# Optimization experiments

Measured on AMD Instinct MI355X. Metric: run time of the kernel, lower is better.

The kernel has to match this reference:

```python
import jax, jax.numpy as jnp
import numpy as np

S, T, B = 32, 64, 64          # sentences, tokens/sentence, batch
V, E, H, G, C = 32000, 128, 128, 128, 5  # vocab, embed, intra hid, inter hid, classes


def _gru_dir(x, h0, Wih, Whh, bih, bhh):
    # x: [T,B,D]; Wih: [3H,D]; Whh: [3H,H]  (PyTorch GRU gate order r,z,n)
    xg = jnp.einsum('tbd,gd->tbg', x, Wih) + bih  # precompute input gates [T,B,3H]
    def step(h, xt):
        gh = h @ Whh.T + bhh
        ir, iz, inn = jnp.split(xt, 3, axis=-1)
        hr, hz, hn = jnp.split(gh, 3, axis=-1)
        r = jax.nn.sigmoid(ir + hr)
        z = jax.nn.sigmoid(iz + hz)
        n = jnp.tanh(inn + r * hn)
        hnew = (1 - z) * n + z * h
        return hnew, hnew
    _, out = jax.lax.scan(step, h0, xg)
    return out  # [T,B,H]


def _bigru(x, Wih, Whh, bih, bhh):
    # x: [T,B,D]; Wih: [2,3H,D] (fwd, bwd). Zero initial state (init_hidden()).
    h0 = jnp.zeros((x.shape[1], Whh.shape[-1]), x.dtype)
    of = _gru_dir(x, h0, Wih[0], Whh[0], bih[0], bhh[0])
    ob = _gru_dir(x[::-1], h0, Wih[1], Whh[1], bih[1], bhh[1])[::-1]
    return jnp.concatenate([of, ob], axis=-1)  # [T,B,2H]


def setup_inputs() -> dict:
    key = jax.random.key(0)
    ks = iter(jax.random.split(key, 20))
    u = lambda k, shp, s: jax.random.uniform(k, shp, jnp.float32, -s, s)
    tokens = jax.random.randint(next(ks), (S, T, B), 0, V)
    return {
        'tokens': tokens,
        'embed_table': jax.random.normal(next(ks), (V, E), jnp.float32),
        # intra biGRU (input E, hidden H)
        'Wih_intra': u(next(ks), (2, 3 * H, E), 0.08),
        'Whh_intra': u(next(ks), (2, 3 * H, H), 0.08),
        'bih_intra': u(next(ks), (2, 3 * H), 0.08),
        'bhh_intra': u(next(ks), (2, 3 * H), 0.08),
        # intra attention
        'W_W_intra': u(next(ks), (2 * H, 2 * H), 0.1),
        'b_intra': u(next(ks), (2 * H,), 0.1),
        'proj_intra': u(next(ks), (2 * H,), 0.1),
        # inter biGRU (input 2H, hidden G)
        'Wih_inter': u(next(ks), (2, 3 * G, 2 * H), 0.08),
        'Whh_inter': u(next(ks), (2, 3 * G, G), 0.08),
        'bih_inter': u(next(ks), (2, 3 * G), 0.08),
        'bhh_inter': u(next(ks), (2, 3 * G), 0.08),
        # inter attention
        'W_W_inter': u(next(ks), (2 * G, 2 * G), 0.1),
        'b_inter': u(next(ks), (2 * G,), 0.1),
        'proj_inter': u(next(ks), (2 * G,), 0.1),
        # final linear
        'W_final': u(next(ks), (C, 2 * G), 0.06),
        'b_final': u(next(ks), (C,), 0.06),
    }


def reference(tokens, embed_table, Wih_intra, Whh_intra, bih_intra, bhh_intra,
              W_W_intra, b_intra, proj_intra, Wih_inter, Whh_inter, bih_inter,
              bhh_inter, W_W_inter, b_inter, proj_inter, W_final, b_final):
    # ---- intra (word-level) per sentence, fresh zero state each sentence ----
    emb = embed_table[tokens]                                   # [S,T,B,E]
    intra_out = jax.vmap(
        lambda xs: _bigru(xs, Wih_intra, Whh_intra, bih_intra, bhh_intra)
    )(emb)                                                      # [S,T,B,2H]
    u1 = jnp.tanh(jnp.einsum('stbh,hk->stbk', intra_out, W_W_intra) + b_intra)
    a1 = jnp.einsum('stbk,k->stb', u1, proj_intra)              # [S,T,B]
    a1 = jax.nn.softmax(a1, axis=1)                             # softmax over tokens
    sent_vecs = jnp.einsum('stb,stbh->sbh', a1, intra_out)      # [S,B,2H]
    # ---- inter (sentence-level) ----
    inter_out = _bigru(sent_vecs, Wih_inter, Whh_inter, bih_inter, bhh_inter)  # [S,B,2G]
    u2 = jnp.tanh(jnp.einsum('sbh,hk->sbk', inter_out, W_W_inter) + b_inter)
    a2 = jnp.einsum('sbk,k->sb', u2, proj_inter)                # NO softmax (faithful to source)
    doc_vec = jnp.einsum('sb,sbh->bh', a2, inter_out)           # [B,2G]
    final_map = doc_vec @ W_final.T + b_final                   # [B,C]
    return final_map
```

## Files before the change

kernel.cpp:

```cpp
#include <hip/hip_runtime.h>

#define S_ 32
#define T_ 64
#define B_ 64
#define V_ 32000
#define E_ 128
#define H_ 128
#define G_ 128
#define C_ 5

typedef short s8v __attribute__((ext_vector_type(8)));
typedef __bf16 b8v __attribute__((ext_vector_type(8)));
typedef float f32x4 __attribute__((ext_vector_type(4)));

template <typename V>
__device__ inline auto mfma_sel(V a, V b, f32x4 c, int)
    -> decltype(__builtin_amdgcn_mfma_f32_16x16x32_bf16(a, b, c, 0, 0, 0)) {
  return __builtin_amdgcn_mfma_f32_16x16x32_bf16(a, b, c, 0, 0, 0);
}
template <typename V>
__device__ inline f32x4 mfma_sel(V a, V b, f32x4 c, long) {
  return __builtin_amdgcn_mfma_f32_16x16x32_bf16(
      __builtin_bit_cast(b8v, a), __builtin_bit_cast(b8v, b), c, 0, 0, 0);
}
__device__ inline f32x4 mfma16(s8v a, s8v b, f32x4 c) { return mfma_sel(a, b, c, 0); }

__device__ inline float b2f(unsigned short u) {
  union { unsigned int i; float f; } v; v.i = ((unsigned int)u) << 16; return v.f;
}
__device__ inline unsigned short f2b(float f) {
  union { float f; unsigned int i; } v; v.f = f;
  return (unsigned short)((v.i + 0x8000u) >> 16);
}
__device__ inline unsigned short f2b_rne(float f) {
  union { float f; unsigned int i; } v; v.f = f;
  unsigned int r = (v.i + 0x7fffu + ((v.i >> 16) & 1u)) >> 16;
  return (unsigned short)r;
}
__device__ inline s8v cvt8(const float* p) {
  const float4 a = *(const float4*)p;
  const float4 b = *(const float4*)(p + 4);
  s8v r;
  r[0] = (short)f2b_rne(a.x); r[1] = (short)f2b_rne(a.y);
  r[2] = (short)f2b_rne(a.z); r[3] = (short)f2b_rne(a.w);
  r[4] = (short)f2b_rne(b.x); r[5] = (short)f2b_rne(b.y);
  r[6] = (short)f2b_rne(b.z); r[7] = (short)f2b_rne(b.w);
  return r;
}
__device__ inline float fsigm(float x) {
  return __builtin_amdgcn_rcpf(1.f + __builtin_amdgcn_exp2f(-1.44269504f * x));
}
__device__ inline float ftanh(float x) {
  return 1.f - 2.f * __builtin_amdgcn_rcpf(1.f + __builtin_amdgcn_exp2f(2.88539008f * x));
}

__device__ inline void lds_barrier() {
  asm volatile("s_waitcnt lgkmcnt(0)\n\ts_barrier" ::: "memory");
}

__global__ __launch_bounds__(256) void k_gtab(
    const float* __restrict__ emb,
    const float* __restrict__ wih,
    const float* __restrict__ bih,
    const float* __restrict__ bhh,
    const float* __restrict__ wwi,
    const float* __restrict__ wihI,
    unsigned short* __restrict__ gtab,
    unsigned short* __restrict__ wta,
    unsigned short* __restrict__ wib)
{
  __shared__ __align__(16) unsigned short smem[64 * 264];
  const int bid = blockIdx.x, tid = threadIdx.x;
  if (bid >= 504) {
    const int cb = bid - 504;
    for (int i = 0; i < 48; ++i) {
      int e4 = cb * 12288 + i * 256 + tid;
      float4 v = *(const float4*)&wihI[(size_t)e4 * 4];
      ushort4 u;
      u.x = f2b_rne(v.x); u.y = f2b_rne(v.y); u.z = f2b_rne(v.z); u.w = f2b_rne(v.w);
      *(ushort4*)&wib[(size_t)e4 * 4] = u;
    }
    return;
  }
  if (bid >= 500) {
    const int n0 = (bid - 500) * 64;
    for (int i = 0; i < 64; ++i) {
      int cid = i * 256 + tid;
      int k = cid >> 6, nl = cid & 63;
      smem[nl * 264 + k] = f2b_rne(wwi[k * 256 + n0 + nl]);
    }
    __syncthreads();
    for (int i = 0; i < 8; ++i) {
      int cid = i * 256 + tid;
      int nl = cid >> 5, k8 = cid & 31;
      *(int4*)&wta[(size_t)(n0 + nl) * 256 + k8 * 8] =
          *(const int4*)&smem[nl * 264 + k8 * 8];
    }
    return;
  }
  const int vbase = bid * 64;
  for (int i = 0; i < 8; ++i) {
    int cid = i * 256 + tid;
    int row = cid >> 5, kc = cid & 31;
    float4 v = *(const float4*)&emb[(size_t)(vbase + row) * 128 + kc * 4];
    ushort4 u;
    u.x = f2b_rne(v.x); u.y = f2b_rne(v.y); u.z = f2b_rne(v.z); u.w = f2b_rne(v.w);
    *(ushort4*)&smem[row * 136 + kc * 4] = u;
  }
  __syncthreads();
  const int w = tid >> 6, l = tid & 63, q = l >> 4, ln = l & 15;
  s8v af[4][4];
  for (int mt = 0; mt < 4; ++mt)
    for (int kf = 0; kf < 4; ++kf)
      af[mt][kf] = *(const s8v*)&smem[(mt * 16 + ln) * 136 + kf * 32 + q * 8];
  for (int nchunk = 0; nchunk < 6; ++nchunk) {
    const int nbase = nchunk * 128;
    s8v bf[2][4];
    float bias[2];
    for (int nt = 0; nt < 2; ++nt) {
      int c = nbase + (w * 2 + nt) * 16 + ln;
      int g = (c < 384) ? c : (c - 384);
      bias[nt] = bih[c] + (g < 256 ? bhh[c] : 0.f);
      for (int kf = 0; kf < 4; ++kf)
        bf[nt][kf] = cvt8(&wih[(size_t)c * 128 + kf * 32 + q * 8]);
    }
    for (int mt = 0; mt < 4; ++mt) {
      for (int nt = 0; nt < 2; ++nt) {
        f32x4 acc = {0.f, 0.f, 0.f, 0.f};
        for (int kf = 0; kf < 4; ++kf) acc = mfma16(af[mt][kf], bf[nt][kf], acc);
        const int col = nbase + (w * 2 + nt) * 16 + ln;
        for (int r = 0; r < 4; ++r) {
          const int row = vbase + mt * 16 + q * 4 + r;
          gtab[(size_t)row * 768 + col] = f2b_rne(acc[r] + bias[nt]);
        }
      }
    }
  }
}

__global__ __launch_bounds__(512) void k_intra(
    const int* __restrict__ tokens,
    const unsigned short* __restrict__ gtab,
    const float* __restrict__ whh,
    const float* __restrict__ bhh,
    unsigned short* __restrict__ iout)
{
  const int bid = blockIdx.x;
  const int s = bid >> 3, dir = (bid >> 2) & 1, bq = bid & 3;
  const int bbase = bq * 16;
  const int tid = threadIdx.x;
  const int w = tid >> 6, l = tid & 63, q = l >> 4, ln = l & 15;
  const int gbase = w * 16, g0 = gbase + q * 4;

  __shared__ __align__(16) unsigned short hb[2][16 * 136];
  __shared__ int tokl[T_ * 16];

  for (int i = tid; i < 2 * 16 * 136; i += 512) ((unsigned short*)hb)[i] = 0;
  for (int i = tid; i < T_ * 16; i += 512) {
    int t = i >> 4, bl = i & 15;
    tokl[i] = tokens[(s * T_ + t) * B_ + bbase + bl] * 768 + dir * 384;
  }

  s8v af[3][4];
  float hbn[4];
  const float* whd = whh + (size_t)dir * (384 * 128);
  const float* bhd = bhh + dir * 384;
  for (int g3 = 0; g3 < 3; ++g3) {
    const int R = g3 * 128 + gbase;
    for (int kf = 0; kf < 4; ++kf)
      af[g3][kf] = cvt8(&whd[(size_t)(R + ln) * 128 + kf * 32 + q * 8]);
  }
  for (int r = 0; r < 4; ++r) hbn[r] = bhd[256 + gbase + q * 4 + r];
  float h[4] = {0.f, 0.f, 0.f, 0.f};
  const int b = bbase + ln;
  __syncthreads();

  ushort4 Xr[4], Xz[4], Xn[4];
#define GLOAD_I(slot, st)                                                   \
  do {                                                                      \
    int tt_ = (st) > (T_ - 1) ? (T_ - 1) : (st);                            \
    int tg_ = dir ? (T_ - 1 - tt_) : tt_;                                   \
    const unsigned short* gp_ =                                             \
        gtab + (size_t)(tokl[tg_ * 16 + ln] + g0);                          \
    Xr[slot] = *(const ushort4*)&gp_[0];                                    \
    Xz[slot] = *(const ushort4*)&gp_[128];                                  \
    Xn[slot] = *(const ushort4*)&gp_[256];                                  \
  } while (0)

  GLOAD_I(0, 0);
  GLOAD_I(1, 1);
  GLOAD_I(2, 2);

  int p = 0;
  for (int it = 0; it < T_ / 4; ++it) {
#pragma unroll
    for (int j = 0; j < 4; ++j) {
      const int step = it * 4 + j;
      const int t = dir ? (T_ - 1 - step) : step;
      GLOAD_I((j + 3) & 3, step + 3);

      s8v bfr[4];
      for (int kf = 0; kf < 4; ++kf)
        bfr[kf] = *(const s8v*)&hb[p][ln * 136 + kf * 32 + q * 8];
      f32x4 c0 = {0.f, 0.f, 0.f, 0.f}, c1 = c0, c2 = c0;
      for (int kf = 0; kf < 4; ++kf) {
        c0 = mfma16(af[0][kf], bfr[kf], c0);
        c1 = mfma16(af[1][kf], bfr[kf], c1);
        c2 = mfma16(af[2][kf], bfr[kf], c2);
      }

      const unsigned short* xrp = (const unsigned short*)&Xr[j];
      const unsigned short* xzp = (const unsigned short*)&Xz[j];
      const unsigned short* xnp = (const unsigned short*)&Xn[j];
      unsigned short hnb[4];
      for (int r = 0; r < 4; ++r) {
        float rr = fsigm(b2f(xrp[r]) + c0[r]);
        float zz = fsigm(b2f(xzp[r]) + c1[r]);
        float nn = ftanh(b2f(xnp[r]) + rr * (c2[r] + hbn[r]));
        float hv = zz * (h[r] - nn) + nn;
        h[r] = hv;
        hnb[r] = f2b(hv);
      }
      ushort4 hv4; hv4.x = hnb[0]; hv4.y = hnb[1]; hv4.z = hnb[2]; hv4.w = hnb[3];
      *(ushort4*)&hb[p ^ 1][ln * 136 + g0] = hv4;
      *(ushort4*)&iout[((size_t)(s * T_ + t) * B_ + b) * 256 + dir * 128 + g0] = hv4;
      lds_barrier();
      p ^= 1;
    }
  }
#undef GLOAD_I
}

__global__ __launch_bounds__(512, 1) void k_attn(
    const unsigned short* __restrict__ iout,
    const unsigned short* __restrict__ wta,
    const float* __restrict__ bint,
    const float* __restrict__ proj,
    const unsigned short* __restrict__ wib,
    const float* __restrict__ bihI,
    const float* __restrict__ bhhI,
    float* __restrict__ xgi)
{
  __shared__ __align__(16) unsigned short wlds[256 * 256];
  __shared__ float lgbuf[8][16];
  __shared__ float lbuf[8][8];
  const int tid = threadIdx.x, bid = blockIdx.x;
  const int s = bid >> 3, b0 = (bid & 7) * 8;
  for (int i = 0; i < 16; ++i) {
    int cid = i * 512 + tid;
    int n = cid >> 5, kc = cid & 31;
    *(int4*)&wlds[n * 256 + ((kc ^ (n & 15)) << 3)] =
        *(const int4*)&wta[(size_t)n * 256 + kc * 8];
  }
  const int w = tid >> 6, l = tid & 63, q = l >> 4, ln = l & 15;
  float bbv[16], ppv[16];
  for (int nt = 0; nt < 16; ++nt) {
    bbv[nt] = bint[nt * 16 + ln];
    ppv[nt] = proj[nt * 16 + ln];
  }
  __syncthreads();

  float O[8][8];
  for (int kf = 0; kf < 8; ++kf)
    for (int j = 0; j < 8; ++j) O[kf][j] = 0.f;
  float l_acc = 0.f;

  for (int tile = 0; tile < 4; ++tile) {
    const int t = (w * 4 + tile) * 2 + (ln >> 3);
    const size_t row = (size_t)((s * T_ + t) * B_ + b0 + (ln & 7));
    s8v af[8];
    for (int kf = 0; kf < 8; ++kf)
      af[kf] = *(const s8v*)&iout[row * 256 + kf * 32 + q * 8];
    float p0 = 0.f, p1 = 0.f, p2 = 0.f, p3 = 0.f;
    for (int nt = 0; nt < 16; ++nt) {
      f32x4 c = {0.f, 0.f, 0.f, 0.f};
      for (int kf = 0; kf < 8; ++kf) {
        s8v bf = *(const s8v*)&wlds[(nt * 16 + ln) * 256 + (((kf * 4 + q) ^ ln) << 3)];
        c = mfma16(af[kf], bf, c);
      }
      p0 += ppv[nt] * ftanh(c[0] + bbv[nt]);
      p1 += ppv[nt] * ftanh(c[1] + bbv[nt]);
      p2 += ppv[nt] * ftanh(c[2] + bbv[nt]);
      p3 += ppv[nt] * ftanh(c[3] + bbv[nt]);
    }
    for (int d = 1; d < 16; d <<= 1) {
      p0 += __shfl_xor(p0, d); p1 += __shfl_xor(p1, d);
      p2 += __shfl_xor(p2, d); p3 += __shfl_xor(p3, d);
    }
    if (ln == 0) {
      lgbuf[w][q * 4 + 0] = p0; lgbuf[w][q * 4 + 1] = p1;
      lgbuf[w][q * 4 + 2] = p2; lgbuf[w][q * 4 + 3] = p3;
    }
    const float lg = lgbuf[w][ln];
    const float e = __builtin_amdgcn_exp2f(1.44269504f * lg);
    l_acc += e;
    for (int kf = 0; kf < 8; ++kf)
      for (int j = 0; j < 8; ++j)
        O[kf][j] += e * b2f((unsigned short)af[kf][j]);
  }
  l_acc += __shfl_xor(l_acc, 8);
  for (int kf = 0; kf < 8; ++kf)
    for (int j = 0; j < 8; ++j) O[kf][j] += __shfl_xor(O[kf][j], 8);
  __syncthreads();
  float* obuf = (float*)wlds;
  unsigned short* svl = (unsigned short*)(((char*)wlds) + 65536);
  if (ln < 8) {
    const int base = w * 2048 + ln * 256 + q * 8;
    for (int kf = 0; kf < 8; ++kf) {
      float4 v0; v0.x = O[kf][0]; v0.y = O[kf][1]; v0.z = O[kf][2]; v0.w = O[kf][3];
      float4 v1; v1.x = O[kf][4]; v1.y = O[kf][5]; v1.z = O[kf][6]; v1.w = O[kf][7];
      *(float4*)&obuf[base + kf * 32]     = v0;
      *(float4*)&obuf[base + kf * 32 + 4] = v1;
    }
    if (q == 0) lbuf[w][ln] = l_acc;
  }
  {
    ushort4 z4; z4.x = 0; z4.y = 0; z4.z = 0; z4.w = 0;
    int rr = 8 + (tid >> 6), cc = (tid & 63) * 4;
    *(ushort4*)&svl[rr * 264 + cc] = z4;
  }
  __syncthreads();
  const int idx = tid * 4;
  const int bb_ = idx >> 8;
  float4 acc; acc.x = 0.f; acc.y = 0.f; acc.z = 0.f; acc.w = 0.f;
  float lsum = 0.f;
  for (int w8 = 0; w8 < 8; ++w8) {
    const float4 v = *(const float4*)&obuf[w8 * 2048 + idx];
    acc.x += v.x; acc.y += v.y; acc.z += v.z; acc.w += v.w;
    lsum += lbuf[w8][bb_];
  }
  const float inv = __builtin_amdgcn_rcpf(lsum);
  ushort4 u;
  u.x = f2b_rne(acc.x * inv); u.y = f2b_rne(acc.y * inv);
  u.z = f2b_rne(acc.z * inv); u.w = f2b_rne(acc.w * inv);
  *(ushort4*)&svl[bb_ * 264 + (idx & 255)] = u;
  __syncthreads();
  s8v afx[8];
  for (int kf = 0; kf < 8; ++kf)
    afx[kf] = *(const s8v*)&svl[ln * 264 + kf * 32 + q * 8];
  for (int nt = 0; nt < 6; ++nt) {
    const int c = w * 96 + nt * 16 + ln;
    const int dirI = (c >= 384) ? 1 : 0;
    const int g = c - dirI * 384;
    const float biasx = bihI[c] + (g < 256 ? bhhI[c] : 0.f);
    f32x4 cacc = {0.f, 0.f, 0.f, 0.f};
    for (int kf = 0; kf < 8; ++kf) {
      s8v bfx = *(const s8v*)&wib[(size_t)c * 256 + kf * 32 + q * 8];
      cacc = mfma16(afx[kf], bfx, cacc);
    }
    if (q < 2) {
      for (int r = 0; r < 4; ++r) {
        const int m = q * 4 + r;
        xgi[((size_t)dirI * 2048 + s * B_ + b0 + m) * 384 + g] = cacc[r] + biasx;
      }
    }
  }
}

__global__ __launch_bounds__(512) void k_inter(
    const float* __restrict__ xgi,
    const float* __restrict__ whh,
    const float* __restrict__ bhh,
    float* __restrict__ io2)
{
  const int bid = blockIdx.x;
  const int dir = bid >> 2, bq = bid & 3, bbase = bq * 16;
  const int tid = threadIdx.x;
  const int w = tid >> 6, l = tid & 63, q = l >> 4, ln = l & 15;
  const int gbase = w * 16, g0 = gbase + q * 4;
  __shared__ __align__(16) unsigned short hb[2][16 * 136];
  for (int i = tid; i < 2 * 16 * 136; i += 512) ((unsigned short*)hb)[i] = 0;
  s8v af[3][4];
  float hbn[4];
  const float* whd = whh + (size_t)dir * (384 * 128);
  const float* bhd = bhh + dir * 384;
  for (int g3 = 0; g3 < 3; ++g3) {
    const int R = g3 * 128 + gbase;
    for (int kf = 0; kf < 4; ++kf)
      af[g3][kf] = cvt8(&whd[(size_t)(R + ln) * 128 + kf * 32 + q * 8]);
  }
  for (int r = 0; r < 4; ++r) hbn[r] = bhd[256 + gbase + q * 4 + r];
  float h[4] = {0.f, 0.f, 0.f, 0.f};
  const int b = bbase + ln;
  __syncthreads();

  float4 Vr[4], Vz[4], Vn[4];
#define GLOAD_S(slot, st)                                                   \
  do {                                                                      \
    int tt_ = (st) > (S_ - 1) ? (S_ - 1) : (st);                            \
    int sg_ = dir ? (S_ - 1 - tt_) : tt_;                                   \
    const float* xp_ = xgi + ((size_t)dir * 2048 + sg_ * 64 + b) * 384 + g0;\
    Vr[slot] = *(const float4*)&xp_[0];                                     \
    Vz[slot] = *(const float4*)&xp_[128];                                   \
    Vn[slot] = *(const float4*)&xp_[256];                                   \
  } while (0)

  GLOAD_S(0, 0);
  GLOAD_S(1, 1);
  GLOAD_S(2, 2);

  int p = 0;
  for (int it = 0; it < S_ / 4; ++it) {
#pragma unroll
    for (int j = 0; j < 4; ++j) {
      const int step = it * 4 + j;
      const int sI = dir ? (S_ - 1 - step) : step;
      GLOAD_S((j + 3) & 3, step + 3);

      s8v bfr[4];
      for (int kf = 0; kf < 4; ++kf)
        bfr[kf] = *(const s8v*)&hb[p][ln * 136 + kf * 32 + q * 8];
      f32x4 c0 = {0.f, 0.f, 0.f, 0.f}, c1 = c0, c2 = c0;
      for (int kf = 0; kf < 4; ++kf) {
        c0 = mfma16(af[0][kf], bfr[kf], c0);
        c1 = mfma16(af[1][kf], bfr[kf], c1);
        c2 = mfma16(af[2][kf], bfr[kf], c2);
      }
      const float irv[4] = {Vr[j].x, Vr[j].y, Vr[j].z, Vr[j].w};
      const float izv[4] = {Vz[j].x, Vz[j].y, Vz[j].z, Vz[j].w};
      const float inv[4] = {Vn[j].x, Vn[j].y, Vn[j].z, Vn[j].w};
      unsigned short hnb[4];
      for (int r = 0; r < 4; ++r) {
        float rr = fsigm(irv[r] + c0[r]);
        float zz = fsigm(izv[r] + c1[r]);
        float nn = ftanh(inv[r] + rr * (c2[r] + hbn[r]));
        float hv = zz * (h[r] - nn) + nn;
        h[r] = hv;
        hnb[r] = f2b(hv);
      }
      ushort4 hv4; hv4.x = hnb[0]; hv4.y = hnb[1]; hv4.z = hnb[2]; hv4.w = hnb[3];
      *(ushort4*)&hb[p ^ 1][ln * 136 + g0] = hv4;
      float4 of4; of4.x = h[0]; of4.y = h[1]; of4.z = h[2]; of4.w = h[3];
      *(float4*)&io2[((size_t)(sI * 64 + b)) * 256 + dir * 128 + g0] = of4;
      lds_barrier();
      p ^= 1;
    }
  }
#undef GLOAD_S
}

__global__ __launch_bounds__(256) void k_attn_i(
    const float* __restrict__ io2,
    const float* __restrict__ wwI,
    const float* __restrict__ bI,
    const float* __restrict__ projI,
    float* __restrict__ a2)
{
  const int bid = blockIdx.x, tid = threadIdx.x;
  const int r0 = bid * 8;
  __shared__ float iol[8 * 256];
  __shared__ float red[4 * 8];
  for (int i = 0; i < 8; ++i) iol[i * 256 + tid] = io2[(size_t)(r0 + i) * 256 + tid];
  __syncthreads();
  float acc[8];
  for (int i = 0; i < 8; ++i) acc[i] = 0.f;
  for (int hh = 0; hh < 256; ++hh) {
    const float wv = wwI[hh * 256 + tid];
    for (int i = 0; i < 8; ++i) acc[i] += wv * iol[i * 256 + hh];
  }
  const float bb = bI[tid], pp = projI[tid];
  float p[8];
  for (int i = 0; i < 8; ++i) p[i] = pp * ftanh(acc[i] + bb);
  for (int d = 1; d < 64; d <<= 1)
    for (int i = 0; i < 8; ++i) p[i] += __shfl_xor(p[i], d);
  const int w = tid >> 6, l = tid & 63;
  if (l == 0)
    for (int i = 0; i < 8; ++i) red[w * 8 + i] = p[i];
  __syncthreads();
  if (tid < 8) a2[r0 + tid] = red[tid] + red[8 + tid] + red[16 + tid] + red[24 + tid];
}

__global__ __launch_bounds__(256) void k_final(
    const float* __restrict__ a2,
    const float* __restrict__ io2,
    const float* __restrict__ wf,
    const float* __restrict__ bfi,
    float* __restrict__ out)
{
  const int b = blockIdx.x, tid = threadIdx.x;
  __shared__ float av[S_];
  __shared__ float dv[256];
  __shared__ float red[4];
  if (tid < S_) av[tid] = a2[tid * 64 + b];
  __syncthreads();
  float acc = 0.f;
  for (int s = 0; s < S_; ++s) acc += av[s] * io2[((size_t)(s * 64 + b)) * 256 + tid];
  dv[tid] = acc;
  __syncthreads();
  for (int c = 0; c < C_; ++c) {
    float pv = wf[c * 256 + tid] * dv[tid];
    for (int d = 1; d < 64; d <<= 1) pv += __shfl_xor(pv, d);
    const int w = tid >> 6, l = tid & 63;
    if (l == 0) red[w] = pv;
    __syncthreads();
    if (tid == 0)
      out[b * C_ + c] = red[0] + red[1] + red[2] + red[3] + bfi[c];
    __syncthreads();
  }
}

extern "C" void kernel_launch(void* const* d_in, const int* in_sizes, int n_in,
                              void* d_out, int out_size, void* d_ws, size_t ws_size,
                              hipStream_t stream) {
  (void)in_sizes; (void)n_in; (void)out_size; (void)ws_size;
  const int*   tokens = (const int*)d_in[0];
  const float* emb    = (const float*)d_in[1];
  const float* wih_a  = (const float*)d_in[2];
  const float* whh_a  = (const float*)d_in[3];
  const float* bih_a  = (const float*)d_in[4];
  const float* bhh_a  = (const float*)d_in[5];
  const float* ww_a   = (const float*)d_in[6];
  const float* b_a    = (const float*)d_in[7];
  const float* proj_a = (const float*)d_in[8];
  const float* wih_i  = (const float*)d_in[9];
  const float* whh_i  = (const float*)d_in[10];
  const float* bih_i  = (const float*)d_in[11];
  const float* bhh_i  = (const float*)d_in[12];
  const float* ww_i   = (const float*)d_in[13];
  const float* b_i    = (const float*)d_in[14];
  const float* proj_i = (const float*)d_in[15];
  const float* w_fin  = (const float*)d_in[16];
  const float* b_fin  = (const float*)d_in[17];

  char* ws = (char*)d_ws;
  unsigned short* gtab = (unsigned short*)(ws + 0);
  unsigned short* wta  = (unsigned short*)(ws + 49152000);
  unsigned short* iout = (unsigned short*)(ws + 49283072);
  unsigned short* wib  = (unsigned short*)(ws + 116391936);
  float* xgi = (float*)(ws + 119537664);
  float* io2 = (float*)(ws + 125829120);
  float* a2  = (float*)(ws + 127926272);

  k_gtab<<<508, 256, 0, stream>>>(emb, wih_a, bih_a, bhh_a, ww_a, wih_i,
                                  gtab, wta, wib);
  k_intra<<<256, 512, 0, stream>>>(tokens, gtab, whh_a, bhh_a, iout);
  k_attn<<<256, 512, 0, stream>>>(iout, wta, b_a, proj_a, wib, bih_i, bhh_i, xgi);
  k_inter<<<8, 512, 0, stream>>>(xgi, whh_i, bhh_i, io2);
  k_attn_i<<<256, 256, 0, stream>>>(io2, ww_i, b_i, proj_i, a2);
  k_final<<<64, 256, 0, stream>>>(a2, io2, w_fin, b_fin, (float*)d_out);
}
```

Baseline: 289.6 us.

## Halve intra-GRU block to 4 waves with two gate tiles each; fuse tail kernels

```diff
diff --git a/kernel.cpp b/kernel.cpp
--- a/kernel.cpp
+++ b/kernel.cpp
@@ -138,7 +138,7 @@
   }
 }
 
-__global__ __launch_bounds__(512) void k_intra(
+__global__ __launch_bounds__(256) void k_intra(
     const int* __restrict__ tokens,
     const unsigned short* __restrict__ gtab,
     const float* __restrict__ whh,
@@ -150,41 +150,50 @@
   const int bbase = bq * 16;
   const int tid = threadIdx.x;
   const int w = tid >> 6, l = tid & 63, q = l >> 4, ln = l & 15;
-  const int gbase = w * 16, g0 = gbase + q * 4;
+  const int gb0 = w * 32;
+  const int g00 = gb0 + q * 4;
+  const int g01 = gb0 + 16 + q * 4;
 
   __shared__ __align__(16) unsigned short hb[2][16 * 136];
   __shared__ int tokl[T_ * 16];
 
-  for (int i = tid; i < 2 * 16 * 136; i += 512) ((unsigned short*)hb)[i] = 0;
-  for (int i = tid; i < T_ * 16; i += 512) {
+  for (int i = tid; i < 2 * 16 * 136; i += 256) ((unsigned short*)hb)[i] = 0;
+  for (int i = tid; i < T_ * 16; i += 256) {
     int t = i >> 4, bl = i & 15;
     tokl[i] = tokens[(s * T_ + t) * B_ + bbase + bl] * 768 + dir * 384;
   }
 
-  s8v af[3][4];
-  float hbn[4];
+  s8v af[3][2][4];
+  float hbn[2][4];
   const float* whd = whh + (size_t)dir * (384 * 128);
   const float* bhd = bhh + dir * 384;
-  for (int g3 = 0; g3 < 3; ++g3) {
-    const int R = g3 * 128 + gbase;
-    for (int kf = 0; kf < 4; ++kf)
-      af[g3][kf] = cvt8(&whd[(size_t)(R + ln) * 128 + kf * 32 + q * 8]);
-  }
-  for (int r = 0; r < 4; ++r) hbn[r] = bhd[256 + gbase + q * 4 + r];
-  float h[4] = {0.f, 0.f, 0.f, 0.f};
+#pragma unroll
+  for (int g3 = 0; g3 < 3; ++g3)
+#pragma unroll
+    for (int hf = 0; hf < 2; ++hf)
+      for (int kf = 0; kf < 4; ++kf)
+        af[g3][hf][kf] =
+            cvt8(&whd[(size_t)(g3 * 128 + gb0 + hf * 16 + ln) * 128 + kf * 32 + q * 8]);
+#pragma unroll
+  for (int hf = 0; hf < 2; ++hf)
+    for (int r = 0; r < 4; ++r)
+      hbn[hf][r] = bhd[256 + gb0 + hf * 16 + q * 4 + r];
+  float h[2][4] = {{0.f, 0.f, 0.f, 0.f}, {0.f, 0.f, 0.f, 0.f}};
   const int b = bbase + ln;
   __syncthreads();
 
-  ushort4 Xr[4], Xz[4], Xn[4];
+  ushort4 Xr[2][4], Xz[2][4], Xn[2][4];
 #define GLOAD_I(slot, st)                                                   \
   do {                                                                      \
     int tt_ = (st) > (T_ - 1) ? (T_ - 1) : (st);                            \
     int tg_ = dir ? (T_ - 1 - tt_) : tt_;                                   \
-    const unsigned short* gp_ =                                             \
-        gtab + (size_t)(tokl[tg_ * 16 + ln] + g0);                          \
-    Xr[slot] = *(const ushort4*)&gp_[0];                                    \
-    Xz[slot] = *(const ushort4*)&gp_[128];                                  \
-    Xn[slot] = *(const ushort4*)&gp_[256];                                  \
+    const unsigned short* gp_ = gtab + (size_t)(tokl[tg_ * 16 + ln]);       \
+    Xr[0][slot] = *(const ushort4*)&gp_[g00];                               \
+    Xz[0][slot] = *(const ushort4*)&gp_[128 + g00];                         \
+    Xn[0][slot] = *(const ushort4*)&gp_[256 + g00];                         \
+    Xr[1][slot] = *(const ushort4*)&gp_[g01];                               \
+    Xz[1][slot] = *(const ushort4*)&gp_[128 + g01];                         \
+    Xn[1][slot] = *(const ushort4*)&gp_[256 + g01];                         \
   } while (0)
 
   GLOAD_I(0, 0);
@@ -202,28 +211,41 @@
       s8v bfr[4];
       for (int kf = 0; kf < 4; ++kf)
         bfr[kf] = *(const s8v*)&hb[p][ln * 136 + kf * 32 + q * 8];
-      f32x4 c0 = {0.f, 0.f, 0.f, 0.f}, c1 = c0, c2 = c0;
+      f32x4 c[3][2];
+#pragma unroll
+      for (int g3 = 0; g3 < 3; ++g3)
+#pragma unroll
+        for (int hf = 0; hf < 2; ++hf) {
+          f32x4 z = {0.f, 0.f, 0.f, 0.f};
+          c[g3][hf] = z;
+        }
       for (int kf = 0; kf < 4; ++kf) {
-        c0 = mfma16(af[0][kf], bfr[kf], c0);
-        c1 = mfma16(af[1][kf], bfr[kf], c1);
-        c2 = mfma16(af[2][kf], bfr[kf], c2);
-      }
-
-      const unsigned short* xrp = (const unsigned short*)&Xr[j];
-      const unsigned short* xzp = (const unsigned short*)&Xz[j];
-      const unsigned short* xnp = (const unsigned short*)&Xn[j];
-      unsigned short hnb[4];
-      for (int r = 0; r < 4; ++r) {
-        float rr = fsigm(b2f(xrp[r]) + c0[r]);
-        float zz = fsigm(b2f(xzp[r]) + c1[r]);
-        float nn = ftanh(b2f(xnp[r]) + rr * (c2[r] + hbn[r]));
-        float hv = zz * (h[r] - nn) + nn;
-        h[r] = hv;
-        hnb[r] = f2b(hv);
-      }
-      ushort4 hv4; hv4.x = hnb[0]; hv4.y = hnb[1]; hv4.z = hnb[2]; hv4.w = hnb[3];
-      *(ushort4*)&hb[p ^ 1][ln * 136 + g0] = hv4;
-      *(ushort4*)&iout[((size_t)(s * T_ + t) * B_ + b) * 256 + dir * 128 + g0] = hv4;
+#pragma unroll
+        for (int g3 = 0; g3 < 3; ++g3)
+#pragma unroll
+          for (int hf = 0; hf < 2; ++hf)
+            c[g3][hf] = mfma16(af[g3][hf][kf], bfr[kf], c[g3][hf]);
+      }
+
+      const size_t rowbase = ((size_t)(s * T_ + t) * B_ + b) * 256 + dir * 128;
+#pragma unroll
+      for (int hf = 0; hf < 2; ++hf) {
+        const unsigned short* xrp = (const unsigned short*)&Xr[hf][j];
+        const unsigned short* xzp = (const unsigned short*)&Xz[hf][j];
+        const unsigned short* xnp = (const unsigned short*)&Xn[hf][j];
+        unsigned short hnb[4];
+        for (int r = 0; r < 4; ++r) {
+          float rr = fsigm(b2f(xrp[r]) + c[0][hf][r]);
+          float zz = fsigm(b2f(xzp[r]) + c[1][hf][r]);
+          float nn = ftanh(b2f(xnp[r]) + rr * (c[2][hf][r] + hbn[hf][r]));
+          float hv = zz * (h[hf][r] - nn) + nn;
+          h[hf][r] = hv;
+          hnb[r] = f2b(hv);
+        }
+        ushort4 hv4; hv4.x = hnb[0]; hv4.y = hnb[1]; hv4.z = hnb[2]; hv4.w = hnb[3];
+        *(ushort4*)&hb[p ^ 1][ln * 136 + gb0 + hf * 16 + q * 4] = hv4;
+        *(ushort4*)&iout[rowbase + gb0 + hf * 16 + q * 4] = hv4;
+      }
       lds_barrier();
       p ^= 1;
     }
@@ -439,62 +461,63 @@
 #undef GLOAD_S
 }
 
-__global__ __launch_bounds__(256) void k_attn_i(
+__global__ __launch_bounds__(512) void k_tail(
     const float* __restrict__ io2,
     const float* __restrict__ wwI,
     const float* __restrict__ bI,
     const float* __restrict__ projI,
-    float* __restrict__ a2)
-{
-  const int bid = blockIdx.x, tid = threadIdx.x;
-  const int r0 = bid * 8;
-  __shared__ float iol[8 * 256];
-  __shared__ float red[4 * 8];
-  for (int i = 0; i < 8; ++i) iol[i * 256 + tid] = io2[(size_t)(r0 + i) * 256 + tid];
-  __syncthreads();
-  float acc[8];
-  for (int i = 0; i < 8; ++i) acc[i] = 0.f;
-  for (int hh = 0; hh < 256; ++hh) {
-    const float wv = wwI[hh * 256 + tid];
-    for (int i = 0; i < 8; ++i) acc[i] += wv * iol[i * 256 + hh];
-  }
-  const float bb = bI[tid], pp = projI[tid];
-  float p[8];
-  for (int i = 0; i < 8; ++i) p[i] = pp * ftanh(acc[i] + bb);
-  for (int d = 1; d < 64; d <<= 1)
-    for (int i = 0; i < 8; ++i) p[i] += __shfl_xor(p[i], d);
-  const int w = tid >> 6, l = tid & 63;
-  if (l == 0)
-    for (int i = 0; i < 8; ++i) red[w * 8 + i] = p[i];
-  __syncthreads();
-  if (tid < 8) a2[r0 + tid] = red[tid] + red[8 + tid] + red[16 + tid] + red[24 + tid];
-}
-
-__global__ __launch_bounds__(256) void k_final(
-    const float* __restrict__ a2,
-    const float* __restrict__ io2,
     const float* __restrict__ wf,
     const float* __restrict__ bfi,
     float* __restrict__ out)
 {
   const int b = blockIdx.x, tid = threadIdx.x;
-  __shared__ float av[S_];
-  __shared__ float dv[256];
-  __shared__ float red[4];
-  if (tid < S_) av[tid] = a2[tid * 64 + b];
-  __syncthreads();
-  float acc = 0.f;
-  for (int s = 0; s < S_; ++s) acc += av[s] * io2[((size_t)(s * 64 + b)) * 256 + tid];
-  dv[tid] = acc;
-  __syncthreads();
+  __shared__ __align__(16) float iol[32][256];
+  __shared__ float pr[8][16];
+  __shared__ float a2s[32];
+  __shared__ float red2[4];
+  for (int i = tid; i < 32 * 256; i += 512) {
+    int ss = i >> 8, d = i & 255;
+    iol[ss][d] = io2[(size_t)(ss * 64 + b) * 256 + d];
+  }
+  __syncthreads();
+  const int k = tid & 255, g = tid >> 8;
+  float acc[16];
+  for (int i = 0; i < 16; ++i) acc[i] = 0.f;
+  for (int h4 = 0; h4 < 64; ++h4) {
+    const float w0 = wwI[(h4 * 4 + 0) * 256 + k];
+    const float w1 = wwI[(h4 * 4 + 1) * 256 + k];
+    const float w2 = wwI[(h4 * 4 + 2) * 256 + k];
+    const float w3 = wwI[(h4 * 4 + 3) * 256 + k];
+    for (int i = 0; i < 16; ++i) {
+      const float4 v = *(const float4*)&iol[g * 16 + i][h4 * 4];
+      acc[i] += w0 * v.x + w1 * v.y + w2 * v.z + w3 * v.w;
+    }
+  }
+  const float bb = bI[k], pp = projI[k];
+  float pv[16];
+  for (int i = 0; i < 16; ++i) pv[i] = pp * ftanh(acc[i] + bb);
+  for (int d = 1; d < 64; d <<= 1)
+    for (int i = 0; i < 16; ++i) pv[i] += __shfl_xor(pv[i], d);
+  if ((tid & 63) == 0)
+    for (int i = 0; i < 16; ++i) pr[tid >> 6][i] = pv[i];
+  __syncthreads();
+  if (tid < 32) {
+    const int g2 = tid >> 4, i2 = tid & 15;
+    a2s[g2 * 16 + i2] = pr[g2 * 4 + 0][i2] + pr[g2 * 4 + 1][i2] +
+                        pr[g2 * 4 + 2][i2] + pr[g2 * 4 + 3][i2];
+  }
+  __syncthreads();
+  float dv = 0.f;
+  if (tid < 256) {
+    for (int ss = 0; ss < 32; ++ss) dv += a2s[ss] * iol[ss][tid];
+  }
   for (int c = 0; c < C_; ++c) {
-    float pv = wf[c * 256 + tid] * dv[tid];
-    for (int d = 1; d < 64; d <<= 1) pv += __shfl_xor(pv, d);
-    const int w = tid >> 6, l = tid & 63;
-    if (l == 0) red[w] = pv;
+    float pvv = (tid < 256) ? wf[c * 256 + tid] * dv : 0.f;
+    for (int d = 1; d < 64; d <<= 1) pvv += __shfl_xor(pvv, d);
+    if (tid < 256 && (tid & 63) == 0) red2[tid >> 6] = pvv;
     __syncthreads();
     if (tid == 0)
-      out[b * C_ + c] = red[0] + red[1] + red[2] + red[3] + bfi[c];
+      out[b * C_ + c] = red2[0] + red2[1] + red2[2] + red2[3] + bfi[c];
     __syncthreads();
   }
 }
@@ -529,13 +552,12 @@
   unsigned short* wib  = (unsigned short*)(ws + 116391936);
   float* xgi = (float*)(ws + 119537664);
   float* io2 = (float*)(ws + 125829120);
-  float* a2  = (float*)(ws + 127926272);
 
   k_gtab<<<508, 256, 0, stream>>>(emb, wih_a, bih_a, bhh_a, ww_a, wih_i,
                                   gtab, wta, wib);
-  k_intra<<<256, 512, 0, stream>>>(tokens, gtab, whh_a, bhh_a, iout);
+  k_intra<<<256, 256, 0, stream>>>(tokens, gtab, whh_a, bhh_a, iout);
   k_attn<<<256, 512, 0, stream>>>(iout, wta, b_a, proj_a, wib, bih_i, bhh_i, xgi);
   k_inter<<<8, 512, 0, stream>>>(xgi, whh_i, bhh_i, io2);
-  k_attn_i<<<256, 256, 0, stream>>>(io2, ww_i, b_i, proj_i, a2);
-  k_final<<<64, 256, 0, stream>>>(a2, io2, w_fin, b_fin, (float*)d_out);
-}
+  k_tail<<<64, 512, 0, stream>>>(io2, ww_i, b_i, proj_i, w_fin, b_fin,
+                                 (float*)d_out);
+}
```

Result: slower. 320.5 us (+10.7%).

## Stage GRU input-gate gathers through LDS and coalesce hidden-state output stores

Applied to the files above, without the earlier changes.

```diff
diff --git a/kernel.cpp b/kernel.cpp
--- a/kernel.cpp
+++ b/kernel.cpp
@@ -153,6 +153,7 @@
   const int gbase = w * 16, g0 = gbase + q * 4;
 
   __shared__ __align__(16) unsigned short hb[2][16 * 136];
+  __shared__ __align__(16) unsigned short xbuf[2][16 * 392];
   __shared__ int tokl[T_ * 16];
 
   for (int i = tid; i < 2 * 16 * 136; i += 512) ((unsigned short*)hb)[i] = 0;
@@ -165,70 +166,96 @@
   float hbn[4];
   const float* whd = whh + (size_t)dir * (384 * 128);
   const float* bhd = bhh + dir * 384;
-  for (int g3 = 0; g3 < 3; ++g3) {
-    const int R = g3 * 128 + gbase;
+  for (int g3 = 0; g3 < 3; ++g3)
     for (int kf = 0; kf < 4; ++kf)
-      af[g3][kf] = cvt8(&whd[(size_t)(R + ln) * 128 + kf * 32 + q * 8]);
-  }
+      af[g3][kf] = cvt8(&whd[(size_t)(g3 * 128 + gbase + ln) * 128 + kf * 32 + q * 8]);
   for (int r = 0; r < 4; ++r) hbn[r] = bhd[256 + gbase + q * 4 + r];
   float h[4] = {0.f, 0.f, 0.f, 0.f};
-  const int b = bbase + ln;
-  __syncthreads();
-
-  ushort4 Xr[4], Xz[4], Xn[4];
-#define GLOAD_I(slot, st)                                                   \
+
+  const bool stager = (w < 6);
+  int sr0 = 0, sof0 = 0, sd0 = 0, sr1 = 0, sof1 = 0, sd1 = 0;
+  {
+    int e0 = w * 1024 + l * 8;
+    int e1 = e0 + 512;
+    sr0 = e0 / 384; sof0 = e0 - sr0 * 384; sd0 = sr0 * 392 + sof0;
+    sr1 = e1 / 384; sof1 = e1 - sr1 * 384; sd1 = sr1 * 392 + sof1;
+  }
+  int4 ldA, ldB;
+#define XLOAD(st)                                                           \
   do {                                                                      \
     int tt_ = (st) > (T_ - 1) ? (T_ - 1) : (st);                            \
     int tg_ = dir ? (T_ - 1 - tt_) : tt_;                                   \
-    const unsigned short* gp_ =                                             \
-        gtab + (size_t)(tokl[tg_ * 16 + ln] + g0);                          \
-    Xr[slot] = *(const ushort4*)&gp_[0];                                    \
-    Xz[slot] = *(const ushort4*)&gp_[128];                                  \
-    Xn[slot] = *(const ushort4*)&gp_[256];                                  \
+    ldA = *(const int4*)&gtab[(size_t)tokl[tg_ * 16 + sr0] + sof0];         \
+    ldB = *(const int4*)&gtab[(size_t)tokl[tg_ * 16 + sr1] + sof1];         \
   } while (0)
-
-  GLOAD_I(0, 0);
-  GLOAD_I(1, 1);
-  GLOAD_I(2, 2);
-
+#define XWRITE(sl)                                                          \
+  do {                                                                      \
+    *(int4*)&xbuf[sl][sd0] = ldA;                                           \
+    *(int4*)&xbuf[sl][sd1] = ldB;                                           \
+  } while (0)
+
+  __syncthreads();
+  if (stager) {
+    XLOAD(0);
+    XWRITE(0);
+    XLOAD(1);
+  }
+  __syncthreads();
+
+  const int xb = ln * 392 + gbase + q * 4;
   int p = 0;
-  for (int it = 0; it < T_ / 4; ++it) {
-#pragma unroll
-    for (int j = 0; j < 4; ++j) {
-      const int step = it * 4 + j;
-      const int t = dir ? (T_ - 1 - step) : step;
-      GLOAD_I((j + 3) & 3, step + 3);
-
-      s8v bfr[4];
-      for (int kf = 0; kf < 4; ++kf)
-        bfr[kf] = *(const s8v*)&hb[p][ln * 136 + kf * 32 + q * 8];
-      f32x4 c0 = {0.f, 0.f, 0.f, 0.f}, c1 = c0, c2 = c0;
-      for (int kf = 0; kf < 4; ++kf) {
-        c0 = mfma16(af[0][kf], bfr[kf], c0);
-        c1 = mfma16(af[1][kf], bfr[kf], c1);
-        c2 = mfma16(af[2][kf], bfr[kf], c2);
-      }
-
-      const unsigned short* xrp = (const unsigned short*)&Xr[j];
-      const unsigned short* xzp = (const unsigned short*)&Xz[j];
-      const unsigned short* xnp = (const unsigned short*)&Xn[j];
-      unsigned short hnb[4];
-      for (int r = 0; r < 4; ++r) {
-        float rr = fsigm(b2f(xrp[r]) + c0[r]);
-        float zz = fsigm(b2f(xzp[r]) + c1[r]);
-        float nn = ftanh(b2f(xnp[r]) + rr * (c2[r] + hbn[r]));
-        float hv = zz * (h[r] - nn) + nn;
-        h[r] = hv;
-        hnb[r] = f2b(hv);
-      }
-      ushort4 hv4; hv4.x = hnb[0]; hv4.y = hnb[1]; hv4.z = hnb[2]; hv4.w = hnb[3];
-      *(ushort4*)&hb[p ^ 1][ln * 136 + g0] = hv4;
-      *(ushort4*)&iout[((size_t)(s * T_ + t) * B_ + b) * 256 + dir * 128 + g0] = hv4;
-      lds_barrier();
-      p ^= 1;
-    }
-  }
-#undef GLOAD_I
+  int tprev = 0;
+  for (int step = 0; step < T_; ++step) {
+    const int t = dir ? (T_ - 1 - step) : step;
+    const int sl = step & 1;
+    if (stager) {
+      XWRITE(sl ^ 1);
+      XLOAD(step + 2);
+    }
+    if (step > 0 && tid < 256) {
+      int row = tid >> 4, kc = tid & 15;
+      int4 v = *(const int4*)&hb[p][row * 136 + kc * 8];
+      *(int4*)&iout[((size_t)(s * T_ + tprev) * B_ + bbase + row) * 256 +
+                    dir * 128 + kc * 8] = v;
+    }
+    s8v bfr[4];
+    for (int kf = 0; kf < 4; ++kf)
+      bfr[kf] = *(const s8v*)&hb[p][ln * 136 + kf * 32 + q * 8];
+    f32x4 c0 = {0.f, 0.f, 0.f, 0.f}, c1 = c0, c2 = c0;
+    for (int kf = 0; kf < 4; ++kf) {
+      c0 = mfma16(af[0][kf], bfr[kf], c0);
+      c1 = mfma16(af[1][kf], bfr[kf], c1);
+      c2 = mfma16(af[2][kf], bfr[kf], c2);
+    }
+    const ushort4 xr = *(const ushort4*)&xbuf[sl][xb];
+    const ushort4 xz = *(const ushort4*)&xbuf[sl][xb + 128];
+    const ushort4 xn = *(const ushort4*)&xbuf[sl][xb + 256];
+    const unsigned short* xrp = (const unsigned short*)&xr;
+    const unsigned short* xzp = (const unsigned short*)&xz;
+    const unsigned short* xnp = (const unsigned short*)&xn;
+    unsigned short hnb[4];
+    for (int r = 0; r < 4; ++r) {
+      float rr = fsigm(b2f(xrp[r]) + c0[r]);
+      float zz = fsigm(b2f(xzp[r]) + c1[r]);
+      float nn = ftanh(b2f(xnp[r]) + rr * (c2[r] + hbn[r]));
+      float hv = zz * (h[r] - nn) + nn;
+      h[r] = hv;
+      hnb[r] = f2b(hv);
+    }
+    ushort4 hv4; hv4.x = hnb[0]; hv4.y = hnb[1]; hv4.z = hnb[2]; hv4.w = hnb[3];
+    *(ushort4*)&hb[p ^ 1][ln * 136 + g0] = hv4;
+    lds_barrier();
+    p ^= 1;
+    tprev = t;
+  }
+  if (tid < 256) {
+    int row = tid >> 4, kc = tid & 15;
+    int4 v = *(const int4*)&hb[p][row * 136 + kc * 8];
+    *(int4*)&iout[((size_t)(s * T_ + tprev) * B_ + bbase + row) * 256 +
+                  dir * 128 + kc * 8] = v;
+  }
+#undef XLOAD
+#undef XWRITE
 }
 
 __global__ __launch_bounds__(512, 1) void k_attn(
```

Result: slower. 300.6 us (+3.8%).
